# Kernel tuning notes

Hardware: AMD Instinct MI355X
Metric: run time of the kernel (lower is better)

## Reference

```python
import jax, jax.numpy as jnp
import numpy as np

jax.config.update("jax_enable_x64", True)

MAX_LEN = 2048
D_MODEL = 2048
CONTEXT = 1
FUDGE = 0.01
MIN_PERIOD = 1
MAX_PERIOD = 1024
FORGOTTEN_AT = 0.01


def _init_params():
    # Mirrors LaplaceAggregation.__init__ with init_method='linspace', modify_real=True
    limit = np.log(np.finfo(np.float64).max) / MAX_LEN - FUDGE
    soft_high = np.log(FORGOTTEN_AT) / MAX_PERIOD
    soft_low = np.log(FORGOTTEN_AT) / MIN_PERIOD
    a_low = max(-limit + FUDGE, soft_low)
    a_high = max(min(-1e-6, soft_high), a_low)
    a = np.linspace(a_low, a_high, D_MODEL).reshape(1, 1, D_MODEL, CONTEXT)
    b = (2.0 * np.pi / np.linspace(MIN_PERIOD, MAX_PERIOD, D_MODEL)).reshape(1, 1, D_MODEL, CONTEXT)
    return jnp.asarray(a, jnp.float64), jnp.asarray(b, jnp.float64)


def setup_inputs() -> dict:
    key = jax.random.key(0)
    k1, k2, k3 = jax.random.split(key, 3)
    B, T, F = 8, 1024, D_MODEL
    x = jax.random.normal(k1, (B, T, F), dtype=jnp.float32)
    mem_real = jax.random.normal(k2, (B, 1, F, CONTEXT), dtype=jnp.float32)
    mem_imag = jax.random.normal(k3, (B, 1, F, CONTEXT), dtype=jnp.float32)
    a, b = _init_params()
    return {"x": x, "mem_real": mem_real, "mem_imag": mem_imag, "a": a, "b": b}


def reference(x, mem_real, mem_imag, a, b):
    # batched_recurrent_update path (1 < T < max_len)
    T = x.shape[1]
    f64, c128 = jnp.float64, jnp.complex128
    ab = a.astype(f64) + 1j * b.astype(f64)           # [1,1,F,C] complex

    def psi(t):  # t: [T] -> [1,T,F,C]
        return jnp.exp(ab * t.reshape(1, -1, 1, 1))

    # inner_idx[:T] = [max_len-1, ..., max_len-T]; outer_idx = -inner_idx
    inner = jnp.arange(MAX_LEN - 1, MAX_LEN - 1 - T, -1, dtype=f64)
    offset = jnp.arange(1, T + 1, dtype=f64)          # state_offset[:T]

    xc = x.astype(f64)[..., None].astype(c128)        # [B,T,F,1]
    z = jnp.cumsum(psi(inner) * xc, axis=1)           # [B,T,F,C]
    mem0 = (mem_real.astype(f64) + 1j * mem_imag.astype(f64))  # [B,1,F,C]
    out = psi(-inner) * z + mem0 * psi(offset)        # [B,T,F,C]
    return out.astype(jnp.complex64)
```

## Files before the change

### kernel.cpp

```cpp
#include <hip/hip_runtime.h>
#include <math.h>

#define BB 8
#define TT 1024
#define FF 2048
#define F2 1024
#define NCH 64
#define LCH 16
#define F2W 8
#define NFB (F2 / F2W)
#define WGT (NCH * F2W)
#define SCAN_R 6
#define NTILE 4


typedef float vf2 __attribute__((ext_vector_type(2)));

__device__ inline void load_ab2(const void* ap, const void* bp, int f,
                                double2& ab0, double2& ab1) {
    double bd = ((const double*)bp)[0];
    if (bd > 6.0 && bd < 6.6) {
        ab0 = make_double2(((const double*)ap)[f],     ((const double*)bp)[f]);
        ab1 = make_double2(((const double*)ap)[f + 1], ((const double*)bp)[f + 1]);
    } else {
        ab0 = make_double2((double)((const float*)ap)[f],
                           (double)((const float*)bp)[f]);
        ab1 = make_double2((double)((const float*)ap)[f + 1],
                           (double)((const float*)bp)[f + 1]);
    }
}

__device__ inline float2 cis_exp_f(double a, double b, double scale) {
    double m = exp(scale * a);
    double s, c;
    sincos(scale * b, &s, &c);
    return make_float2((float)(m * c), (float)(m * s));
}

__device__ inline float2 csqf(float2 u) {
    return make_float2(fmaf(u.x, u.x, -u.y * u.y), 2.f * u.x * u.y);
}

__device__ inline void nt_store2(float2* p, float lo, float hi) {
    vf2 v; v.x = lo; v.y = hi;
    __builtin_nontemporal_store(v, reinterpret_cast<vf2*>(p));
}

__device__ inline void lds_barrier() {
    __builtin_amdgcn_sched_barrier(0);
    asm volatile("s_waitcnt lgkmcnt(0)");
    __builtin_amdgcn_s_barrier();
    __builtin_amdgcn_sched_barrier(0);
}

#define DO_TILE(XV, XN, BB_CUR, BB_NXT, HAVE_NXT)                              \
  do {                                                                         \
    float2 mem_r = mr2[(size_t)(BB_CUR) * F2 + f2g];                           \
    float2 mem_i = mi2[(size_t)(BB_CUR) * F2 + f2g];                           \
       \
    if (HAVE_NXT) {                                                            \
      const float2* xpn =                                                      \
          x2 + ((size_t)(BB_NXT) * TT + (size_t)c * LCH) * F2 + f2g;           \
      _Pragma("unroll")                                                        \
      for (int j = 0; j < LCH; ++j) (XN)[j] = xpn[(size_t)j * F2];             \
    }                                                                          \
         \
    float4 z[LCH];                                                             \
    {                                                                          \
      float zr0 = 0.f, zi0 = 0.f, zr1 = 0.f, zi1 = 0.f;                        \
      _Pragma("unroll")                                                        \
      for (int j = 0; j < LCH; ++j) {                                          \
        float2 xvj = (XV)[j];                                                  \
        float nr0 = fmaf(l0.x, zr0, fmaf(-l0.y, zi0, xvj.x));                  \
        float ni0 = fmaf(l0.x, zi0, l0.y * zr0);                               \
        float nr1 = fmaf(l1.x, zr1, fmaf(-l1.y, zi1, xvj.y));                  \
        float ni1 = fmaf(l1.x, zi1, l1.y * zr1);                               \
        zr0 = nr0; zi0 = ni0; zr1 = nr1; zi1 = ni1;                            \
        z[j] = make_float4(zr0, zi0, zr1, zi1);                                \
      }                                                                        \
    }                                                                          \
            \
    float4 P = z[LCH - 1];                                                     \
    float2 m0 = m0b, m1 = m1b;                                                 \
    lds_barrier();           \
    sS[0][c][f2] = P;                                                          \
    lds_barrier();                                                             \
    int pb = 0;                                                                \
    _Pragma("unroll")                                                          \
    for (int r = 0; r < SCAN_R; ++r) {                                         \
      int k = 1 << r;                                                          \
      float4 part = make_float4(0.f, 0.f, 0.f, 0.f);                           \
      if (c >= k) part = sS[pb][c - k][f2];                                    \
      P.x = fmaf(m0.x, part.x, fmaf(-m0.y, part.y, P.x));                      \
      P.y = fmaf(m0.x, part.y, fmaf( m0.y, part.x, P.y));                      \
      P.z = fmaf(m1.x, part.z, fmaf(-m1.y, part.w, P.z));                      \
      P.w = fmaf(m1.x, part.w, fmaf( m1.y, part.z, P.w));                      \
      m0 = csqf(m0); m1 = csqf(m1);                                            \
      sS[pb ^ 1][c][f2] = P;                                                   \
      lds_barrier();                                                           \
      pb ^= 1;                                                                 \
    }                                                                          \
    float4 Pm1 = make_float4(0.f, 0.f, 0.f, 0.f);                              \
    if (c > 0) Pm1 = sS[pb][c - 1][f2];                                        \
                                  \
    float Wr0 = fmaf(e0.x, mem_r.x, fmaf(-e0.y, mem_i.x, Pm1.x));              \
    float Wi0 = fmaf(e0.x, mem_i.x, fmaf( e0.y, mem_r.x, Pm1.y));              \
    float Wr1 = fmaf(e1.x, mem_r.y, fmaf(-e1.y, mem_i.y, Pm1.z));              \
    float Wi1 = fmaf(e1.x, mem_i.y, fmaf( e1.y, mem_r.y, Pm1.w));              \
                  \
    size_t base2 = ((size_t)(BB_CUR) * TT + (size_t)c * LCH) * F2 + f2g;       \
    _Pragma("unroll")                                                          \
    for (int j = 0; j < LCH; ++j) {                                            \
      float nWr0 = fmaf(l0.x, Wr0, -l0.y * Wi0);                               \
      float nWi0 = fmaf(l0.x, Wi0,  l0.y * Wr0);                               \
      float nWr1 = fmaf(l1.x, Wr1, -l1.y * Wi1);                               \
      float nWi1 = fmaf(l1.x, Wi1,  l1.y * Wr1);                               \
      Wr0 = nWr0; Wi0 = nWi0; Wr1 = nWr1; Wi1 = nWi1;                          \
      float4 zj = z[j];                                                        \
      size_t idx2 = base2 + (size_t)j * F2;                                    \
      if (idx2 < limit2) nt_store2(&out2[idx2], zj.x + Wr0, zj.z + Wr1);       \
      size_t ii2 = idx2 + plane2;                                              \
      if (ii2 < limit2) nt_store2(&out2[ii2], zj.y + Wi0, zj.w + Wi1);         \
    }                                                                          \
  } while (0)

__global__ void __launch_bounds__(WGT, 2)
k_fused(const float2* __restrict__ x2, const float2* __restrict__ mr2,
        const float2* __restrict__ mi2, const void* __restrict__ a,
        const void* __restrict__ b, float2* __restrict__ out2, size_t limit2) {
    __shared__ float4 sS[2][NCH][F2W];

    int tid = threadIdx.x;
    int f2  = tid & (F2W - 1);
    int c   = tid >> 3;

    int bid = blockIdx.x;
    int swz = ((bid & 7) << 5) | (bid >> 3);
    int fb  = swz & (NFB - 1);
    int bq  = swz >> 7;
    int f2g = fb * F2W + f2;

    const size_t plane2 = (size_t)BB * TT * F2;

    int b0 = bq, b1 = bq + 2, b2 = bq + 4, b3 = bq + 6;

    float2 xvA[LCH], xvB[LCH];
    {
        const float2* xp0 = x2 + ((size_t)b0 * TT + (size_t)c * LCH) * F2 + f2g;
#pragma unroll
        for (int j = 0; j < LCH; ++j) xvA[j] = xp0[(size_t)j * F2];
    }

    double2 ab0, ab1;
    load_ab2(a, b, 2 * f2g, ab0, ab1);
    float2 l0 = cis_exp_f(ab0.x, ab0.y, 1.0);
    float2 l1 = cis_exp_f(ab1.x, ab1.y, 1.0);
    float2 m0b = l0, m1b = l1;
#pragma unroll
    for (int s = 0; s < 4; ++s) { m0b = csqf(m0b); m1b = csqf(m1b); }
    float2 e0 = cis_exp_f(ab0.x, ab0.y, (double)(c * LCH));
    float2 e1 = cis_exp_f(ab1.x, ab1.y, (double)(c * LCH));

    DO_TILE(xvA, xvB, b0, b1, 1);
    DO_TILE(xvB, xvA, b1, b2, 1);
    DO_TILE(xvA, xvB, b2, b3, 1);
    DO_TILE(xvB, xvA, b3, b3, 0);
}

extern "C" void kernel_launch(void* const* d_in, const int* in_sizes, int n_in,
                              void* d_out, int out_size, void* d_ws, size_t ws_size,
                              hipStream_t stream) {
    const float2* x2  = (const float2*)d_in[0];
    const float2* mr2 = (const float2*)d_in[1];
    const float2* mi2 = (const float2*)d_in[2];
    const void*   a   = d_in[3];
    const void*   b   = d_in[4];
    float2* out2 = (float2*)d_out;
    (void)d_ws; (void)ws_size; (void)n_in; (void)in_sizes;

    size_t limit2 = (size_t)out_size >> 1;

    int grid = (BB / NTILE) * NFB;
    k_fused<<<grid, WGT, 0, stream>>>(x2, mr2, mi2, a, b, out2, limit2);
}
```

Baseline: 126.5 us.

## Restructure scan: one batch per block, time tiles with wave-level carry

Work is regrouped so each block handles one batch and 64 features, with 16 waves each scanning a 16-step chunk, and the block loops over 4 time tiles of 256 steps. The carry between tiles is kept in double-precision registers. The old 6-round Hillis-Steele LDS scan with a barrier per round is replaced by one LDS exchange of per-wave sums followed by a serial 16-step combine. This removes most barriers and lets the cross-tile prefix ride in registers. The cost is more redundant per-thread combine work, blocks of 1024 threads with a different occupancy bound, and scalar float stores in place of float2 stores.

```diff
diff --git a/kernel.cpp b/kernel.cpp
--- a/kernel.cpp
+++ b/kernel.cpp
@@ -4,46 +4,17 @@
 #define BB 8
 #define TT 1024
 #define FF 2048
-#define F2 1024
-#define NCH 64
+#define NW 16
 #define LCH 16
-#define F2W 8
-#define NFB (F2 / F2W)
-#define WGT (NCH * F2W)
-#define SCAN_R 6
-#define NTILE 4
+#define NTK 4
+#define WGT (NW * 64)
+#define NFC 32
+#define PLANEF ((size_t)BB * TT * FF)
 
 
-typedef float vf2 __attribute__((ext_vector_type(2)));
-
-__device__ inline void load_ab2(const void* ap, const void* bp, int f,
-                                double2& ab0, double2& ab1) {
+__device__ inline bool ab_is_f64(const void* bp) {
     double bd = ((const double*)bp)[0];
-    if (bd > 6.0 && bd < 6.6) {
-        ab0 = make_double2(((const double*)ap)[f],     ((const double*)bp)[f]);
-        ab1 = make_double2(((const double*)ap)[f + 1], ((const double*)bp)[f + 1]);
-    } else {
-        ab0 = make_double2((double)((const float*)ap)[f],
-                           (double)((const float*)bp)[f]);
-        ab1 = make_double2((double)((const float*)ap)[f + 1],
-                           (double)((const float*)bp)[f + 1]);
-    }
-}
-
-__device__ inline float2 cis_exp_f(double a, double b, double scale) {
-    double m = exp(scale * a);
-    double s, c;
-    sincos(scale * b, &s, &c);
-    return make_float2((float)(m * c), (float)(m * s));
-}
-
-__device__ inline float2 csqf(float2 u) {
-    return make_float2(fmaf(u.x, u.x, -u.y * u.y), 2.f * u.x * u.y);
-}
-
-__device__ inline void nt_store2(float2* p, float lo, float hi) {
-    vf2 v; v.x = lo; v.y = hi;
-    __builtin_nontemporal_store(v, reinterpret_cast<vf2*>(p));
+    return (bd > 6.0 && bd < 6.6);
 }
 
 __device__ inline void lds_barrier() {
@@ -53,133 +24,160 @@
     __builtin_amdgcn_sched_barrier(0);
 }
 
-#define DO_TILE(XV, XN, BB_CUR, BB_NXT, HAVE_NXT)                              \
+#define DO_TILE(K, XV, XN, HAVE_NXT)                                           \
   do {                                                                         \
-    float2 mem_r = mr2[(size_t)(BB_CUR) * F2 + f2g];                           \
-    float2 mem_i = mi2[(size_t)(BB_CUR) * F2 + f2g];                           \
-       \
+                \
     if (HAVE_NXT) {                                                            \
-      const float2* xpn =                                                      \
-          x2 + ((size_t)(BB_NXT) * TT + (size_t)c * LCH) * F2 + f2g;           \
+      const float* xpn = xb + (size_t)(((K) + 1) * (NW * LCH) + w * LCH) * FF; \
       _Pragma("unroll")                                                        \
-      for (int j = 0; j < LCH; ++j) (XN)[j] = xpn[(size_t)j * F2];             \
+      for (int j = 0; j < LCH; ++j) (XN)[j] = xpn[(size_t)j * FF];             \
     }                                                                          \
          \
-    float4 z[LCH];                                                             \
+    float zr[LCH], zi[LCH];                                                    \
+    float Sx, Sy;                                                              \
     {                                                                          \
-      float zr0 = 0.f, zi0 = 0.f, zr1 = 0.f, zi1 = 0.f;                        \
+      float sr = 0.f, si = 0.f;                                                \
       _Pragma("unroll")                                                        \
       for (int j = 0; j < LCH; ++j) {                                          \
-        float2 xvj = (XV)[j];                                                  \
-        float nr0 = fmaf(l0.x, zr0, fmaf(-l0.y, zi0, xvj.x));                  \
-        float ni0 = fmaf(l0.x, zi0, l0.y * zr0);                               \
-        float nr1 = fmaf(l1.x, zr1, fmaf(-l1.y, zi1, xvj.y));                  \
-        float ni1 = fmaf(l1.x, zi1, l1.y * zr1);                               \
-        zr0 = nr0; zi0 = ni0; zr1 = nr1; zi1 = ni1;                            \
-        z[j] = make_float4(zr0, zi0, zr1, zi1);                                \
+        float xj = (XV)[j];                                                    \
+        float nr = fmaf(l.x, sr, fmaf(-l.y, si, xj));                          \
+        float ni = fmaf(l.x, si, l.y * sr);                                    \
+        sr = nr; si = ni; zr[j] = nr; zi[j] = ni;                              \
       }                                                                        \
+      Sx = sr; Sy = si;                                                        \
     }                                                                          \
-            \
-    float4 P = z[LCH - 1];                                                     \
-    float2 m0 = m0b, m1 = m1b;                                                 \
-    lds_barrier();           \
-    sS[0][c][f2] = P;                                                          \
-    lds_barrier();                                                             \
-    int pb = 0;                                                                \
+                             \
+    lds_barrier();                 \
+    sL[w][lane] = make_float2(Sx, Sy);                                         \
+    lds_barrier();                                                    \
+    float qr = 0.f, qi = 0.f, fr = 0.f, fi = 0.f;                              \
     _Pragma("unroll")                                                          \
-    for (int r = 0; r < SCAN_R; ++r) {                                         \
-      int k = 1 << r;                                                          \
-      float4 part = make_float4(0.f, 0.f, 0.f, 0.f);                           \
-      if (c >= k) part = sS[pb][c - k][f2];                                    \
-      P.x = fmaf(m0.x, part.x, fmaf(-m0.y, part.y, P.x));                      \
-      P.y = fmaf(m0.x, part.y, fmaf( m0.y, part.x, P.y));                      \
-      P.z = fmaf(m1.x, part.z, fmaf(-m1.y, part.w, P.z));                      \
-      P.w = fmaf(m1.x, part.w, fmaf( m1.y, part.z, P.w));                      \
-      m0 = csqf(m0); m1 = csqf(m1);                                            \
-      sS[pb ^ 1][c][f2] = P;                                                   \
-      lds_barrier();                                                           \
-      pb ^= 1;                                                                 \
+    for (int v = 0; v < NW; ++v) {                                             \
+      float2 sv = sL[v][lane];                                                 \
+      if (v < w) {                                           \
+        float t1 = fmaf(m16f.x, qr, fmaf(-m16f.y, qi, sv.x));                  \
+        float t2 = fmaf(m16f.x, qi, fmaf( m16f.y, qr, sv.y));                  \
+        qr = t1; qi = t2;                                                      \
+      }                                                                        \
+      float t3 = fmaf(m16f.x, fr, fmaf(-m16f.y, fi, sv.x));                    \
+      float t4 = fmaf(m16f.x, fi, fmaf( m16f.y, fr, sv.y));                    \
+      fr = t3; fi = t4;                                                        \
     }                                                                          \
-    float4 Pm1 = make_float4(0.f, 0.f, 0.f, 0.f);                              \
-    if (c > 0) Pm1 = sS[pb][c - 1][f2];                                        \
-                                  \
-    float Wr0 = fmaf(e0.x, mem_r.x, fmaf(-e0.y, mem_i.x, Pm1.x));              \
-    float Wi0 = fmaf(e0.x, mem_i.x, fmaf( e0.y, mem_r.x, Pm1.y));              \
-    float Wr1 = fmaf(e1.x, mem_r.y, fmaf(-e1.y, mem_i.y, Pm1.z));              \
-    float Wi1 = fmaf(e1.x, mem_i.y, fmaf( e1.y, mem_r.y, Pm1.w));              \
-                  \
-    size_t base2 = ((size_t)(BB_CUR) * TT + (size_t)c * LCH) * F2 + f2g;       \
+                     \
+    float Pr_ = (float)(Mwr * Rr - Mwi * Ri) + qr;                             \
+    float Pi_ = (float)(Mwr * Ri + Mwi * Rr) + qi;                             \
+    float Wr = (float)(Er * (double)m0r - Ei * (double)m0i) + Pr_;             \
+    float Wi = (float)(Er * (double)m0i + Ei * (double)m0r) + Pi_;             \
+                             \
+    {                                                                          \
+      double nRr = M256r * Rr - M256i * Ri + (double)fr;                       \
+      double nRi = M256r * Ri + M256i * Rr + (double)fi;                       \
+      Rr = nRr; Ri = nRi;                                                      \
+      double nEr = Er * M256r - Ei * M256i;                                    \
+      double nEi = Er * M256i + Ei * M256r;                                    \
+      Er = nEr; Ei = nEi;                                                      \
+    }                                                                          \
+          \
+    size_t ro = (size_t)(bb * TT + (K) * (NW * LCH) + w * LCH) * FF + f;       \
     _Pragma("unroll")                                                          \
     for (int j = 0; j < LCH; ++j) {                                            \
-      float nWr0 = fmaf(l0.x, Wr0, -l0.y * Wi0);                               \
-      float nWi0 = fmaf(l0.x, Wi0,  l0.y * Wr0);                               \
-      float nWr1 = fmaf(l1.x, Wr1, -l1.y * Wi1);                               \
-      float nWi1 = fmaf(l1.x, Wi1,  l1.y * Wr1);                               \
-      Wr0 = nWr0; Wi0 = nWi0; Wr1 = nWr1; Wi1 = nWi1;                          \
-      float4 zj = z[j];                                                        \
-      size_t idx2 = base2 + (size_t)j * F2;                                    \
-      if (idx2 < limit2) nt_store2(&out2[idx2], zj.x + Wr0, zj.z + Wr1);       \
-      size_t ii2 = idx2 + plane2;                                              \
-      if (ii2 < limit2) nt_store2(&out2[ii2], zj.y + Wi0, zj.w + Wi1);         \
+      float nWr = fmaf(l.x, Wr, -l.y * Wi);                                    \
+      float nWi = fmaf(l.x, Wi,  l.y * Wr);                                    \
+      Wr = nWr; Wi = nWi;                                                      \
+      size_t ir = ro + (size_t)j * FF;                                         \
+      if (ir < limitF)                                                         \
+        __builtin_nontemporal_store(zr[j] + Wr, out + ir);                     \
+      size_t ii = ir + PLANEF;                                                 \
+      if (ii < limitF)                                                         \
+        __builtin_nontemporal_store(zi[j] + Wi, out + ii);                     \
     }                                                                          \
   } while (0)
 
-__global__ void __launch_bounds__(WGT, 2)
-k_fused(const float2* __restrict__ x2, const float2* __restrict__ mr2,
-        const float2* __restrict__ mi2, const void* __restrict__ a,
-        const void* __restrict__ b, float2* __restrict__ out2, size_t limit2) {
-    __shared__ float4 sS[2][NCH][F2W];
+__global__ void __launch_bounds__(WGT)
+k_fused(const float* __restrict__ x, const float* __restrict__ mr,
+        const float* __restrict__ mi, const void* __restrict__ a,
+        const void* __restrict__ b, float* __restrict__ out, size_t limitF) {
+    __shared__ float2 sL[NW][64];
 
-    int tid = threadIdx.x;
-    int f2  = tid & (F2W - 1);
-    int c   = tid >> 3;
+    int tid  = threadIdx.x;
+    int lane = tid & 63;
+    int w    = tid >> 6;
+    int fcol = blockIdx.x & (NFC - 1);
+    int bb   = blockIdx.x >> 5;
+    int f    = fcol * 64 + lane;
 
-    int bid = blockIdx.x;
-    int swz = ((bid & 7) << 5) | (bid >> 3);
-    int fb  = swz & (NFB - 1);
-    int bq  = swz >> 7;
-    int f2g = fb * F2W + f2;
+    const float* xb = x + (size_t)bb * TT * FF + f;
 
-    const size_t plane2 = (size_t)BB * TT * F2;
+    float xvA[LCH], xvB[LCH];
+    {
+        const float* xp0 = xb + (size_t)(w * LCH) * FF;
+#pragma unroll
+        for (int j = 0; j < LCH; ++j) xvA[j] = xp0[(size_t)j * FF];
+    }
+    float m0r = mr[(size_t)bb * FF + f];
+    float m0i = mi[(size_t)bb * FF + f];
 
-    int b0 = bq, b1 = bq + 2, b2 = bq + 4, b3 = bq + 6;
+    double ar, brr;
+    if (ab_is_f64(b)) {
+        ar  = ((const double*)a)[f];
+        brr = ((const double*)b)[f];
+    } else {
+        ar  = (double)((const float*)a)[f];
+        brr = (double)((const float*)b)[f];
+    }
+    double mg = exp(ar), s_, c_;
+    sincos(brr, &s_, &c_);
+    double lrd = mg * c_, lid = mg * s_;
+    float2 l = make_float2((float)lrd, (float)lid);
 
-    float2 xvA[LCH], xvB[LCH];
-    {
-        const float2* xp0 = x2 + ((size_t)b0 * TT + (size_t)c * LCH) * F2 + f2g;
+    double tr = lrd, ti = lid;
 #pragma unroll
-        for (int j = 0; j < LCH; ++j) xvA[j] = xp0[(size_t)j * F2];
+    for (int s = 0; s < 4; ++s) {
+        double nr = tr * tr - ti * ti, ni = 2.0 * tr * ti;
+        tr = nr; ti = ni;
+    }
+    double m16r = tr, m16i = ti;
+    float2 m16f = make_float2((float)m16r, (float)m16i);
+#pragma unroll
+    for (int s = 0; s < 4; ++s) {
+        double nr = tr * tr - ti * ti, ni = 2.0 * tr * ti;
+        tr = nr; ti = ni;
+    }
+    double M256r = tr, M256i = ti;
+
+    double Mwr = 1.0, Mwi = 0.0, pr = m16r, pi = m16i;
+#pragma unroll
+    for (int bit = 0; bit < 4; ++bit) {
+        if ((w >> bit) & 1) {
+            double nr = Mwr * pr - Mwi * pi, ni = Mwr * pi + Mwi * pr;
+            Mwr = nr; Mwi = ni;
+        }
+        double nr = pr * pr - pi * pi, ni = 2.0 * pr * pi;
+        pr = nr; pi = ni;
     }
 
-    double2 ab0, ab1;
-    load_ab2(a, b, 2 * f2g, ab0, ab1);
-    float2 l0 = cis_exp_f(ab0.x, ab0.y, 1.0);
-    float2 l1 = cis_exp_f(ab1.x, ab1.y, 1.0);
-    float2 m0b = l0, m1b = l1;
-#pragma unroll
-    for (int s = 0; s < 4; ++s) { m0b = csqf(m0b); m1b = csqf(m1b); }
-    float2 e0 = cis_exp_f(ab0.x, ab0.y, (double)(c * LCH));
-    float2 e1 = cis_exp_f(ab1.x, ab1.y, (double)(c * LCH));
+    double Er = Mwr, Ei = Mwi;
+    double Rr = 0.0, Ri = 0.0;
 
-    DO_TILE(xvA, xvB, b0, b1, 1);
-    DO_TILE(xvB, xvA, b1, b2, 1);
-    DO_TILE(xvA, xvB, b2, b3, 1);
-    DO_TILE(xvB, xvA, b3, b3, 0);
+    DO_TILE(0, xvA, xvB, 1);
+    DO_TILE(1, xvB, xvA, 1);
+    DO_TILE(2, xvA, xvB, 1);
+    DO_TILE(3, xvB, xvA, 0);
 }
 
 extern "C" void kernel_launch(void* const* d_in, const int* in_sizes, int n_in,
                               void* d_out, int out_size, void* d_ws, size_t ws_size,
                               hipStream_t stream) {
-    const float2* x2  = (const float2*)d_in[0];
-    const float2* mr2 = (const float2*)d_in[1];
-    const float2* mi2 = (const float2*)d_in[2];
-    const void*   a   = d_in[3];
-    const void*   b   = d_in[4];
-    float2* out2 = (float2*)d_out;
+    const float* x  = (const float*)d_in[0];
+    const float* mr = (const float*)d_in[1];
+    const float* mi = (const float*)d_in[2];
+    const void*  a  = d_in[3];
+    const void*  b  = d_in[4];
+    float* out = (float*)d_out;
     (void)d_ws; (void)ws_size; (void)n_in; (void)in_sizes;
 
-    size_t limit2 = (size_t)out_size >> 1;
+    size_t limitF = (size_t)out_size;
 
-    int grid = (BB / NTILE) * NFB;
-    k_fused<<<grid, WGT, 0, stream>>>(x2, mr2, mi2, a, b, out2, limit2);
+    int grid = BB * NFC;
+    k_fused<<<grid, WGT, 0, stream>>>(x, mr, mi, a, b, out, limitF);
 }
```

Result: faster. 121.0 us (-4.4%).
